# Optimization experiments

Hardware: AMD Instinct MI355X
Metric: run time of the kernel (lower is better)

Reference implementation:

```python
import jax, jax.numpy as jnp
import numpy as np

N, E, B = 50000, 800000, 512
DIN, H, A, BT = 128, 256, 40, 5


def _ln(h, g, b):
    m = jnp.mean(h, -1, keepdims=True)
    v = jnp.mean((h - m) ** 2, -1, keepdims=True)
    return (h - m) * jax.lax.rsqrt(v + 1e-5) * g + b


def _gcn(x, w, b, src, dst, n):
    # PyG GCNConv: add self-loops, symmetric D^-1/2 (A+I) D^-1/2 normalization
    h = x @ w
    loop = jnp.arange(n)
    s = jnp.concatenate([src, loop])
    d = jnp.concatenate([dst, loop])
    deg = jax.ops.segment_sum(jnp.ones(s.shape[0], h.dtype), d, num_segments=n)
    dinv = jax.lax.rsqrt(jnp.maximum(deg, 1.0))
    coef = (dinv[s] * dinv[d])[:, None]
    return jax.ops.segment_sum(coef * h[s], d, num_segments=n) + b


def _mlp2(x, w1, b1, w2, b2):
    return jax.nn.relu(x @ w1 + b1) @ w2 + b2


def _mlp3(x, w1, b1, w2, b2, w3, b3):
    h = jax.nn.relu(x @ w1 + b1)
    h = jax.nn.relu(h @ w2 + b2)
    return h @ w3 + b3


def setup_inputs() -> dict:
    key = jax.random.key(0)
    ks = iter(jax.random.split(key, 64))
    p = lambda shape: jax.random.normal(next(ks), shape, jnp.float32) * 0.05
    inp = {}
    inp["x"] = jax.random.normal(next(ks), (N, DIN), jnp.float32)
    inp["edge_index"] = jax.random.randint(next(ks), (2, E), 0, N)
    inp["batch"] = jnp.sort(jax.random.randint(next(ks), (N,), 0, B))
    inp["new_node_indices"] = jax.random.randint(next(ks), (B,), 0, N)
    inp["focus_node_indices"] = jax.random.randint(next(ks), (B,), 0, N)
    inp["num_graphs"] = B
    inp["conv_w0"] = p((DIN, H)); inp["conv_b0"] = p((H,))
    inp["conv_w1"] = p((H, H)); inp["conv_b1"] = p((H,))
    inp["conv_w2"] = p((H, H)); inp["conv_b2"] = p((H,))
    for i in range(3):
        inp[f"ln_g{i}"] = jnp.ones((H,), jnp.float32)
        inp[f"ln_b{i}"] = jnp.zeros((H,), jnp.float32)
    inp["res_w0"] = p((DIN, H)); inp["res_b0"] = p((H,))
    inp["stop_w1"] = p((H, H)); inp["stop_b1"] = p((H,))
    inp["stop_w2"] = p((H, 1)); inp["stop_b2"] = p((1,))
    inp["addn_w1"] = p((H, H)); inp["addn_b1"] = p((H,))
    inp["addn_w2"] = p((H, A)); inp["addn_b2"] = p((A,))
    inp["addb_w1"] = p((H, H)); inp["addb_b1"] = p((H,))
    inp["addb_w2"] = p((H, BT)); inp["addb_b2"] = p((BT,))
    inp["edge_w1"] = p((2 * H, H)); inp["edge_b1"] = p((H,))
    inp["edge_w2"] = p((H, H // 2)); inp["edge_b2"] = p((H // 2,))
    inp["edge_w3"] = p((H // 2, 1)); inp["edge_b3"] = p((1,))
    inp["bond_w1"] = p((2 * H, H)); inp["bond_b1"] = p((H,))
    inp["bond_w2"] = p((H, H // 2)); inp["bond_b2"] = p((H // 2,))
    inp["bond_w3"] = p((H // 2, BT)); inp["bond_b3"] = p((BT,))
    return inp


def reference(x, edge_index, batch, new_node_indices, focus_node_indices, num_graphs,
              conv_w0, conv_b0, conv_w1, conv_b1, conv_w2, conv_b2,
              ln_g0, ln_b0, ln_g1, ln_b1, ln_g2, ln_b2,
              res_w0, res_b0,
              stop_w1, stop_b1, stop_w2, stop_b2,
              addn_w1, addn_b1, addn_w2, addn_b2,
              addb_w1, addb_b1, addb_w2, addb_b2,
              edge_w1, edge_b1, edge_w2, edge_b2, edge_w3, edge_b3,
              bond_w1, bond_b1, bond_w2, bond_b2, bond_w3, bond_b3):
    n = x.shape[0]
    src, dst = edge_index[0], edge_index[1]
    conv_params = [(conv_w0, conv_b0), (conv_w1, conv_b1), (conv_w2, conv_b2)]
    ln_params = [(ln_g0, ln_b0), (ln_g1, ln_b1), (ln_g2, ln_b2)]
    h = x
    for i in range(3):
        h_in = h
        cw, cb = conv_params[i]
        lg, lb = ln_params[i]
        h = _gcn(h, cw, cb, src, dst, n)
        h = jax.nn.relu(_ln(h, lg, lb))  # dropout: eval mode (identity)
        res = h_in @ res_w0 + res_b0 if i == 0 else h_in
        h = h + res
    node_embeddings = h  # [N, H]
    # global mean pool over graphs
    counts = jax.ops.segment_sum(jnp.ones(n, h.dtype), batch, num_segments=num_graphs)
    graph_embedding = jax.ops.segment_sum(node_embeddings, batch, num_segments=num_graphs) / jnp.maximum(counts, 1.0)[:, None]
    stop_logits = _mlp2(graph_embedding, stop_w1, stop_b1, stop_w2, stop_b2)
    add_node_logits = _mlp2(graph_embedding, addn_w1, addn_b1, addn_w2, addn_b2)
    add_bond_logits = _mlp2(node_embeddings[focus_node_indices], addb_w1, addb_b1, addb_w2, addb_b2)
    # pair each node with its graph's newly added node
    new_node_embeddings = node_embeddings[new_node_indices]  # [B, H]
    pair = jnp.concatenate([node_embeddings, new_node_embeddings[batch]], axis=1)  # [N, 2H]
    edge_selection_logits = _mlp3(pair, edge_w1, edge_b1, edge_w2, edge_b2, edge_w3, edge_b3)
    bond_type_logits = _mlp3(pair, bond_w1, bond_b1, bond_w2, bond_b2, bond_w3, bond_b3)
    return (stop_logits, add_node_logits, add_bond_logits, node_embeddings,
            edge_selection_logits, bond_type_logits)
```

## Files before the change

### kernel.cpp

```cpp
#include <hip/hip_runtime.h>

typedef short bf16x8 __attribute__((ext_vector_type(8)));
typedef float f32x4 __attribute__((ext_vector_type(4)));
typedef unsigned short u16;
typedef u16 u16x4 __attribute__((ext_vector_type(4)));
typedef u16 u16x8 __attribute__((ext_vector_type(8)));

__device__ __forceinline__ float bf2f(u16 u) {
  union { float f; unsigned int i; } x; x.i = ((unsigned int)u) << 16; return x.f;
}
__device__ __forceinline__ u16 f2bf(float f) {
  union { float f; unsigned int i; } x; x.f = f;
  unsigned int r = x.i + 0x7fffu + ((x.i >> 16) & 1u);
  return (u16)(r >> 16);
}
__device__ __forceinline__ void st_out_(void* out, size_t idx, float v, int f32) {
  if (f32) ((float*)out)[idx] = v;
  else ((u16*)out)[idx] = f2bf(v);
}
__device__ __forceinline__ void gl_lds(const u16* g, u16* l) {
  __builtin_amdgcn_global_load_lds(
      (const __attribute__((address_space(1))) unsigned int*)g,
      (__attribute__((address_space(3))) unsigned int*)l, 16, 0, 0);
}

__global__ void k_detect(const u16* __restrict__ xx, int* flag) {
  int j = threadIdx.x;
  u16 u = xx[2 * j];
  int ex = (u >> 7) & 0xFF;
  int insane = (u != 0) && (ex < 100 || ex > 140);
  unsigned long long m = __ballot(insane);
  if (j == 0) flag[0] = (__popcll(m) > 8) ? 1 : 0;
}

__global__ void k_cvt_big(const void* __restrict__ src, u16* __restrict__ dst, int n,
                          const int* __restrict__ flag) {
  int i = blockIdx.x * 256 + threadIdx.x;
  if (i >= n) return;
  dst[i] = (*flag) ? f2bf(((const float*)src)[i]) : ((const u16*)src)[i];
}

#define NSEG 38
struct Cvt { const void* src[NSEG]; int off[NSEG + 1]; };
__global__ void k_cvt_all(Cvt c, u16* __restrict__ dst, int total, const int* __restrict__ flag) {
  int i = blockIdx.x * 256 + threadIdx.x;
  if (i >= total) return;
  int s = 0;
  #pragma unroll 1
  while (i >= c.off[s + 1]) s++;
  int j = i - c.off[s];
  dst[i] = (*flag) ? f2bf(((const float*)c.src[s])[j]) : ((const u16*)c.src[s])[j];
}

struct Tr { const u16* src[8]; u16* dst[8]; int lk[8]; int nc[8]; int off[9]; };
__global__ void k_tr_all(Tr c, int total) {
  int i = blockIdx.x * 256 + threadIdx.x;
  if (i >= total) return;
  int s = 0;
  #pragma unroll 1
  while (i >= c.off[s + 1]) s++;
  int j = i - c.off[s];
  int K = 1 << c.lk[s];
  int nrow = j >> c.lk[s], k = j & (K - 1);
  c.dst[s][j] = c.src[s][k * c.nc[s] + nrow];
}

__global__ void k_init(int* deg, int* cursor, int n) {
  int i = blockIdx.x * 256 + threadIdx.x;
  if (i < n) { deg[i] = 1; cursor[i] = 0; }
}
__global__ void k_deg(const int* __restrict__ dst, int* deg, int e) {
  int i = blockIdx.x * 256 + threadIdx.x;
  if (i < e) atomicAdd(&deg[dst[i]], 1);
}
__global__ void k_dinv(const int* __restrict__ deg, float* dinv, int n) {
  int i = blockIdx.x * 256 + threadIdx.x;
  if (i < n) dinv[i] = rsqrtf((float)deg[i]);
}
#define SCB 4096
__global__ __launch_bounds__(256) void k_scanA(const int* __restrict__ deg, int* bsum, int n) {
  int b = blockIdx.x, t = threadIdx.x;
  int base = b * SCB;
  int s = 0;
  for (int j = t; j < SCB; j += 256) { int i = base + j; s += (i < n) ? deg[i] - 1 : 0; }
  int l = t & 63, wid = t >> 6;
  #pragma unroll
  for (int o = 32; o; o >>= 1) s += __shfl_xor(s, o);
  __shared__ int red[4];
  if (l == 0) red[wid] = s;
  __syncthreads();
  if (t == 0) bsum[b] = red[0] + red[1] + red[2] + red[3];
}
__global__ void k_scanB(int* bsum, int nb, int* off, int n) {
  if (threadIdx.x == 0) {
    int c = 0;
    for (int i = 0; i < nb; i++) { int v = bsum[i]; bsum[i] = c; c += v; }
    off[n] = c;
  }
}
__global__ __launch_bounds__(256) void k_scanC(const int* __restrict__ deg, const int* __restrict__ bsum,
                                               int* off, int n) {
  int b = blockIdx.x, t = threadIdx.x;
  int base = b * SCB + t * 16;
  int loc[16]; int s = 0;
  #pragma unroll
  for (int j = 0; j < 16; j++) { int i = base + j; loc[j] = s; s += (i < n) ? deg[i] - 1 : 0; }
  int l = t & 63, wid = t >> 6;
  int incl = s;
  #pragma unroll
  for (int o = 1; o < 64; o <<= 1) { int y = __shfl_up(incl, o); if (l >= o) incl += y; }
  int excl = incl - s;
  __shared__ int ws[4];
  if (l == 63) ws[wid] = incl;
  __syncthreads();
  int woff = 0;
  for (int w = 0; w < wid; w++) woff += ws[w];
  int pre = bsum[b] + woff + excl;
  #pragma unroll
  for (int j = 0; j < 16; j++) { int i = base + j; if (i < n) off[i] = pre + loc[j]; }
}
__global__ void k_csr(const int* __restrict__ src, const int* __restrict__ dst,
                      const int* __restrict__ off, int* cursor, int* csr_src, int e) {
  int i = blockIdx.x * 256 + threadIdx.x;
  if (i >= e) return;
  int d = dst[i], s = src[i];
  int slot = atomicAdd(&cursor[d], 1);
  csr_src[off[d] + slot] = s;
}

template <int EPI>
__global__ __launch_bounds__(256) void gemm_k(
    const u16* __restrict__ A, int lda,
    const u16* __restrict__ Bt,
    u16* __restrict__ C, int ldc,
    int M, int K, int NC,
    const u16* __restrict__ colbias,
    const float* __restrict__ rowbias, int rbld, const int* __restrict__ rowmap) {
  __shared__ u16 As[2][128 * 64];
  __shared__ u16 Bs[2][128 * 64];
  const int t = threadIdx.x;
  const int m0 = blockIdx.x * 128;
  const int n0 = blockIdx.y * 128;
  const int wid = t >> 6, l = t & 63;
  const int wr = wid >> 1, wc = wid & 1;
  const int lr = l & 15, lg = l >> 4;
  const int srow = l >> 3, gc = l & 7;
  const int sg = gc ^ srow;

  auto stage = [&](int buf, int k0) {
    #pragma unroll
    for (int j = 0; j < 4; j++) {
      int row = wid * 32 + j * 8 + srow;
      int ga = m0 + row; if (ga >= M) ga = M - 1;
      gl_lds(A + (size_t)ga * lda + k0 + sg * 8, &As[buf][row * 64 + gc * 8]);
      gl_lds(Bt + (size_t)(n0 + row) * K + k0 + sg * 8, &Bs[buf][row * 64 + gc * 8]);
    }
  };

  f32x4 acc[4][4] = {};
  const int nT = K >> 6;
  stage(0, 0);
  asm volatile("s_waitcnt vmcnt(0)" ::: "memory");
  __builtin_amdgcn_s_barrier();
  int cur = 0;
  for (int kt = 0; kt < nT; kt++) {
    if (kt + 1 < nT) stage(cur ^ 1, (kt + 1) << 6);
    #pragma unroll
    for (int ks = 0; ks < 2; ks++) {
      const int gp = ((ks * 4 + lg) ^ (lr & 7)) * 8;
      bf16x8 af[4], bfr[4];
      #pragma unroll
      for (int mi = 0; mi < 4; mi++)
        af[mi] = *reinterpret_cast<const bf16x8*>(&As[cur][(wr * 64 + mi * 16 + lr) * 64 + gp]);
      #pragma unroll
      for (int ni = 0; ni < 4; ni++)
        bfr[ni] = *reinterpret_cast<const bf16x8*>(&Bs[cur][(wc * 64 + ni * 16 + lr) * 64 + gp]);
      #pragma unroll
      for (int mi = 0; mi < 4; mi++)
        #pragma unroll
        for (int ni = 0; ni < 4; ni++)
          acc[mi][ni] = __builtin_amdgcn_mfma_f32_16x16x32_bf16(af[mi], bfr[ni], acc[mi][ni], 0, 0, 0);
    }
    if (kt + 1 < nT) {
      asm volatile("s_waitcnt vmcnt(0)" ::: "memory");
      __builtin_amdgcn_s_barrier();
      cur ^= 1;
    }
  }
  #pragma unroll
  for (int mi = 0; mi < 4; mi++) {
    #pragma unroll
    for (int ni = 0; ni < 4; ni++) {
      int col = n0 + wc * 64 + ni * 16 + lr;
      float cbv = 0.f;
      if (EPI == 1 || EPI == 2) cbv = bf2f(colbias[col]);
      #pragma unroll
      for (int r = 0; r < 4; r++) {
        int row = m0 + wr * 64 + mi * 16 + lg * 4 + r;
        if (row < M) {
          float v = acc[mi][ni][r];
          if (EPI == 1 || EPI == 2) v += cbv;
          if (EPI == 3) v += rowbias[(size_t)rowmap[row] * rbld + col];
          if (EPI == 2 || EPI == 3) v = fmaxf(v, 0.f);
          C[(size_t)row * ldc + col] = f2bf(v);
        }
      }
    }
  }
}

__global__ __launch_bounds__(256, 6) void k_agg(
    const u16* __restrict__ hw, const u16* __restrict__ cb,
    const u16* __restrict__ lng, const u16* __restrict__ lnb,
    const u16* __restrict__ res, const float* __restrict__ dinv,
    const int* __restrict__ off, const int* __restrict__ csr_src,
    u16* __restrict__ hout, int n) {
  int l = threadIdx.x & 63;
  int v = blockIdx.x * 4 + (threadIdx.x >> 6);
  if (v >= n) return;
  const int half = l >> 5;
  const int c0 = (l & 31) * 8;
  float a[8] = {0, 0, 0, 0, 0, 0, 0, 0};
  int s = off[v], e = off[v + 1];
  int i = s;
  for (; i + 7 < e; i += 8) {
    int u0 = csr_src[i + half],     u1 = csr_src[i + 2 + half];
    int u2 = csr_src[i + 4 + half], u3 = csr_src[i + 6 + half];
    float w0 = dinv[u0], w1 = dinv[u1], w2 = dinv[u2], w3 = dinv[u3];
    u16x8 r0 = *reinterpret_cast<const u16x8*>(hw + (size_t)u0 * 256 + c0);
    u16x8 r1 = *reinterpret_cast<const u16x8*>(hw + (size_t)u1 * 256 + c0);
    u16x8 r2 = *reinterpret_cast<const u16x8*>(hw + (size_t)u2 * 256 + c0);
    u16x8 r3 = *reinterpret_cast<const u16x8*>(hw + (size_t)u3 * 256 + c0);
    #pragma unroll
    for (int j = 0; j < 8; j++)
      a[j] += w0 * bf2f(r0[j]) + w1 * bf2f(r1[j]) + w2 * bf2f(r2[j]) + w3 * bf2f(r3[j]);
  }
  for (; i < e; i += 2) {
    int idx = i + half;
    if (idx < e) {
      int u = csr_src[idx];
      float w = dinv[u];
      u16x8 r = *reinterpret_cast<const u16x8*>(hw + (size_t)u * 256 + c0);
      #pragma unroll
      for (int j = 0; j < 8; j++) a[j] += w * bf2f(r[j]);
    }
  }
  #pragma unroll
  for (int j = 0; j < 8; j++) a[j] += __shfl_xor(a[j], 32);
  float dv = dinv[v];
  u16x8 sv = *reinterpret_cast<const u16x8*>(hw + (size_t)v * 256 + c0);
  u16x8 cbv = *reinterpret_cast<const u16x8*>(cb + c0);
  float sum = 0.f;
  #pragma unroll
  for (int j = 0; j < 8; j++) {
    a[j] = dv * (dv * bf2f(sv[j]) + a[j]) + bf2f(cbv[j]);
    sum += a[j];
  }
  #pragma unroll
  for (int o = 16; o; o >>= 1) sum += __shfl_xor(sum, o);
  float mean = sum * (1.f / 256.f);
  float vs = 0.f;
  #pragma unroll
  for (int j = 0; j < 8; j++) { float d = a[j] - mean; vs += d * d; }
  #pragma unroll
  for (int o = 16; o; o >>= 1) vs += __shfl_xor(vs, o);
  float rs = rsqrtf(vs * (1.f / 256.f) + 1e-5f);
  u16x8 gv = *reinterpret_cast<const u16x8*>(lng + c0);
  u16x8 bv = *reinterpret_cast<const u16x8*>(lnb + c0);
  u16x8 rv = *reinterpret_cast<const u16x8*>(res + (size_t)v * 256 + c0);
  u16x8 ov;
  #pragma unroll
  for (int j = 0; j < 8; j++)
    ov[j] = f2bf(fmaxf((a[j] - mean) * rs * bf2f(gv[j]) + bf2f(bv[j]), 0.f) + bf2f(rv[j]));
  if (half == 0)
    *reinterpret_cast<u16x8*>(hout + (size_t)v * 256 + c0) = ov;
}

__global__ __launch_bounds__(256) void k_pool(const u16* __restrict__ h, const int* __restrict__ batch,
                                              int n, float* gemb) {
  int g = blockIdx.x, c = threadIdx.x;
  int lo = 0, hi = n;
  while (lo < hi) { int mid = (lo + hi) >> 1; if (batch[mid] < g) lo = mid + 1; else hi = mid; }
  int s = lo;
  lo = s; hi = n;
  while (lo < hi) { int mid = (lo + hi) >> 1; if (batch[mid] < g + 1) lo = mid + 1; else hi = mid; }
  int e = lo;
  float acc = 0.f;
  for (int i = s; i < e; i++) acc += bf2f(h[(size_t)i * 256 + c]);
  int cnt = e - s; if (cnt < 1) cnt = 1;
  gemb[g * 256 + c] = acc / (float)cnt;
}

__global__ __launch_bounds__(256) void k_glin(const u16* __restrict__ h, const int* __restrict__ nidx,
                                              const u16* __restrict__ W, const u16* __restrict__ b1,
                                              float* g1, int ld, int ofs) {
  int b = blockIdx.x, t = threadIdx.x;
  __shared__ float sin_[256];
  sin_[t] = bf2f(h[(size_t)nidx[b] * 256 + t]);
  __syncthreads();
  float acc = bf2f(b1[t]);
  for (int k = 0; k < 256; k++) acc += sin_[k] * bf2f(W[k * 256 + t]);
  g1[(size_t)b * ld + ofs + t] = acc;
}

template <int OUTD>
__global__ __launch_bounds__(256) void k_mlp2(const float* __restrict__ inf32,
                                              const u16* __restrict__ inbf, const int* __restrict__ idx,
                                              const u16* __restrict__ W1, const u16* __restrict__ b1,
                                              const u16* __restrict__ W2, const u16* __restrict__ b2,
                                              void* __restrict__ out, size_t obase,
                                              const int* __restrict__ flag) {
  int b = blockIdx.x, t = threadIdx.x;
  __shared__ float sin_[256];
  __shared__ float sh[256];
  sin_[t] = inf32 ? inf32[b * 256 + t] : bf2f(inbf[(size_t)idx[b] * 256 + t]);
  __syncthreads();
  float acc = bf2f(b1[t]);
  for (int k = 0; k < 256; k++) acc += sin_[k] * bf2f(W1[k * 256 + t]);
  sh[t] = fmaxf(acc, 0.f);
  __syncthreads();
  if (t < OUTD) {
    float a2 = bf2f(b2[t]);
    for (int k = 0; k < 256; k++) a2 += sh[k] * bf2f(W2[k * OUTD + t]);
    st_out_(out, obase + (size_t)b * OUTD + t, a2, *flag);
  }
}

__global__ __launch_bounds__(256) void k_final(const u16* __restrict__ t2e, const u16* __restrict__ t2b,
                                               const u16* __restrict__ w3e, const u16* __restrict__ b3e,
                                               const u16* __restrict__ w3b, const u16* __restrict__ b3b,
                                               void* __restrict__ out, size_t oe, size_t ob, int M,
                                               const int* __restrict__ flag) {
  int r = blockIdx.x * 4 + (threadIdx.x >> 6);
  int l = threadIdx.x & 63;
  if (r >= M) return;
  float p[6] = {0, 0, 0, 0, 0, 0};
  #pragma unroll
  for (int j = 0; j < 2; j++) {
    int k = l * 2 + j;
    float te = bf2f(t2e[(size_t)r * 128 + k]);
    float tb = bf2f(t2b[(size_t)r * 128 + k]);
    p[0] += te * bf2f(w3e[k]);
    #pragma unroll
    for (int q = 0; q < 5; q++) p[1 + q] += tb * bf2f(w3b[k * 5 + q]);
  }
  #pragma unroll
  for (int q = 0; q < 6; q++)
    #pragma unroll
    for (int o = 32; o; o >>= 1) p[q] += __shfl_xor(p[q], o);
  if (l == 0) {
    int f32 = *flag;
    st_out_(out, oe + r, p[0] + bf2f(b3e[0]), f32);
    #pragma unroll
    for (int q = 0; q < 5; q++)
      st_out_(out, ob + (size_t)r * 5 + q, p[1 + q] + bf2f(b3b[q]), f32);
  }
}

__global__ void k_emit8(const u16* __restrict__ src, void* __restrict__ out, size_t obase, int n8,
                        const int* __restrict__ flag) {
  int i = blockIdx.x * 256 + threadIdx.x;
  if (i >= n8) return;
  u16x8 v = reinterpret_cast<const u16x8*>(src)[i];
  if (*flag) {
    float4* fo = (float4*)((float*)out + obase);
    float4 lo, hi;
    lo.x = bf2f(v[0]); lo.y = bf2f(v[1]); lo.z = bf2f(v[2]); lo.w = bf2f(v[3]);
    hi.x = bf2f(v[4]); hi.y = bf2f(v[5]); hi.z = bf2f(v[6]); hi.w = bf2f(v[7]);
    fo[(size_t)i * 2] = lo; fo[(size_t)i * 2 + 1] = hi;
  } else {
    reinterpret_cast<u16x8*>((u16*)out + obase)[i] = v;
  }
}

extern "C" void kernel_launch(void* const* d_in, const int* in_sizes, int n_in,
                              void* d_out, int out_size, void* d_ws, size_t ws_size,
                              hipStream_t stream) {
  const int N = in_sizes[0] / 128;
  const int E = in_sizes[1] / 2;
  const int B = in_sizes[3];

  const int* ei    = (const int*)d_in[1];
  const int* srcp  = ei;
  const int* dstp  = ei + E;
  const int* batch = (const int*)d_in[2];
  const int* newi  = (const int*)d_in[3];
  const int* focus = (const int*)d_in[4];

  const size_t o_stop = 0;
  const size_t o_addn = (size_t)B;
  const size_t o_addb = (size_t)B + (size_t)B * 40;
  const size_t o_emb  = o_addb + (size_t)B * 5;
  const size_t o_esel = o_emb + (size_t)N * 256;
  const size_t o_bond = o_esel + (size_t)N;

  char* p = (char*)d_ws;
  auto alloc = [&](size_t bytes) -> void* {
    void* r = (void*)p;
    p += (bytes + 255) & ~(size_t)255;
    return r;
  };
  int* flag = (int*)alloc(4);
  static const int seg_din[NSEG] = {6,7,8,9,10,11, 12,13,14,15,16,17, 18,19,
                                    20,21,22,23, 24,25,26,27, 28,29,30,31,
                                    32,33,34,35,36,37, 38,39,40,41,42,43};
  static const int seg_len[NSEG] = {32768,256,65536,256,65536,256, 256,256,256,256,256,256,
                                    32768,256, 65536,256,256,1, 65536,256,10240,40,
                                    65536,256,1280,5, 131072,256,32768,128,128,1,
                                    131072,256,32768,128,640,5};
  int wtotal = 0;
  int seg_off[NSEG + 1];
  for (int i = 0; i < NSEG; i++) { seg_off[i] = wtotal; wtotal += seg_len[i]; }
  seg_off[NSEG] = wtotal;
  u16* wbf = (u16*)alloc((size_t)wtotal * 2);
  u16* wt_cw0 = (u16*)alloc(256 * 128 * 2);
  u16* wt_cw1 = (u16*)alloc(256 * 256 * 2);
  u16* wt_cw2 = (u16*)alloc(256 * 256 * 2);
  u16* wt_res = (u16*)alloc(256 * 128 * 2);
  u16* wt_t1  = (u16*)alloc(512 * 256 * 2);
  u16* wt_e2  = (u16*)alloc(128 * 256 * 2);
  u16* wt_b2  = (u16*)alloc(128 * 256 * 2);
  int*   deg     = (int*)alloc((size_t)N * 4);
  int*   cursor  = (int*)alloc((size_t)N * 4);
  int*   off     = (int*)alloc((size_t)(N + 1) * 4);
  float* dinv    = (float*)alloc((size_t)N * 4);
  int*   bsum    = (int*)alloc(64 * 4);
  float* gemb    = (float*)alloc((size_t)B * 256 * 4);
  float* g1full  = (float*)alloc((size_t)B * 512 * 4);
  int*   csr_src = (int*)alloc((size_t)E * 4);
  u16*   xbf     = (u16*)alloc((size_t)N * 128 * 2);
  u16*   P1      = (u16*)alloc((size_t)N * 256 * 2);
  u16*   P2      = (u16*)alloc((size_t)N * 256 * 2);
  u16*   P3      = (u16*)alloc((size_t)N * 256 * 2);

  auto wseg = [&](int i) -> u16* { return wbf + seg_off[i]; };
  u16 *cw0 = wseg(0), *cb0 = wseg(1), *cw1 = wseg(2), *cb1 = wseg(3), *cw2 = wseg(4), *cb2 = wseg(5);
  u16 *lg0 = wseg(6), *lb0 = wseg(7), *lg1 = wseg(8), *lb1 = wseg(9), *lg2 = wseg(10), *lb2 = wseg(11);
  u16 *rw0 = wseg(12), *rb0 = wseg(13);
  u16 *sw1 = wseg(14), *sb1 = wseg(15), *sw2 = wseg(16), *sb2 = wseg(17);
  u16 *aw1 = wseg(18), *ab1 = wseg(19), *aw2 = wseg(20), *ab2 = wseg(21);
  u16 *bw1 = wseg(22), *bb1 = wseg(23), *bw2 = wseg(24), *bb2 = wseg(25);
  u16 *ew1 = wseg(26), *eb1 = wseg(27), *ew2 = wseg(28), *eb2 = wseg(29), *ew3 = wseg(30), *eb3 = wseg(31);
  u16 *qw1 = wseg(32), *qb1 = wseg(33), *qw2 = wseg(34), *qb2 = wseg(35), *qw3 = wseg(36), *qb3 = wseg(37);

  k_detect<<<1, 64, 0, stream>>>((const u16*)d_in[0], flag);
  k_cvt_big<<<(N * 128 + 255) / 256, 256, 0, stream>>>(d_in[0], xbf, N * 128, flag);
  Cvt cd;
  for (int i = 0; i < NSEG; i++) cd.src[i] = d_in[seg_din[i]];
  for (int i = 0; i <= NSEG; i++) cd.off[i] = seg_off[i];
  k_cvt_all<<<(wtotal + 255) / 256, 256, 0, stream>>>(cd, wbf, wtotal, flag);

  const int NB = (N + 255) / 256;
  const int EBk = (E + 255) / 256;
  const int NBS = (N + SCB - 1) / SCB;

  k_init<<<NB, 256, 0, stream>>>(deg, cursor, N);
  k_deg<<<EBk, 256, 0, stream>>>(dstp, deg, E);
  k_dinv<<<NB, 256, 0, stream>>>(deg, dinv, N);
  k_scanA<<<NBS, 256, 0, stream>>>(deg, bsum, N);
  k_scanB<<<1, 64, 0, stream>>>(bsum, NBS, off, N);
  k_scanC<<<NBS, 256, 0, stream>>>(deg, bsum, off, N);
  k_csr<<<EBk, 256, 0, stream>>>(srcp, dstp, off, cursor, csr_src, E);

  {
    Tr td;
    const u16* ts[8] = {cw0, cw1, cw2, rw0, ew1, qw1, ew2, qw2};
    u16* tdst[8] = {wt_cw0, wt_cw1, wt_cw2, wt_res, wt_t1, wt_t1 + 256 * 256, wt_e2, wt_b2};
    int tlk[8] = {7, 8, 8, 7, 8, 8, 8, 8};
    int tnc[8] = {256, 256, 256, 256, 256, 256, 128, 128};
    int tlen[8] = {32768, 65536, 65536, 32768, 65536, 65536, 32768, 32768};
    int tot = 0;
    for (int i = 0; i < 8; i++) {
      td.src[i] = ts[i]; td.dst[i] = tdst[i]; td.lk[i] = tlk[i]; td.nc[i] = tnc[i];
      td.off[i] = tot; tot += tlen[i];
    }
    td.off[8] = tot;
    k_tr_all<<<(tot + 255) / 256, 256, 0, stream>>>(td, tot);
  }

  dim3 g256((N + 127) / 128, 2);
  dim3 g512((N + 127) / 128, 4);
  dim3 g128((N + 127) / 128, 1);
  const int AGB = (N + 3) / 4;

  gemm_k<1><<<g256, 256, 0, stream>>>(xbf, 128, wt_res, P1, 256, N, 128, 256, rb0, nullptr, 0, nullptr);
  gemm_k<0><<<g256, 256, 0, stream>>>(xbf, 128, wt_cw0, P2, 256, N, 128, 256, nullptr, nullptr, 0, nullptr);
  k_agg<<<AGB, 256, 0, stream>>>(P2, cb0, lg0, lb0, P1, dinv, off, csr_src, P3, N);
  gemm_k<0><<<g256, 256, 0, stream>>>(P3, 256, wt_cw1, P2, 256, N, 256, 256, nullptr, nullptr, 0, nullptr);
  k_agg<<<AGB, 256, 0, stream>>>(P2, cb1, lg1, lb1, P3, dinv, off, csr_src, P1, N);
  gemm_k<0><<<g256, 256, 0, stream>>>(P1, 256, wt_cw2, P2, 256, N, 256, 256, nullptr, nullptr, 0, nullptr);
  k_agg<<<AGB, 256, 0, stream>>>(P2, cb2, lg2, lb2, P1, dinv, off, csr_src, P3, N);

  k_emit8<<<(N * 256 / 8 + 255) / 256, 256, 0, stream>>>(P3, d_out, o_emb, N * 256 / 8, flag);

  k_pool<<<B, 256, 0, stream>>>(P3, batch, N, gemb);
  k_glin<<<B, 256, 0, stream>>>(P3, newi, ew1 + 256 * 256, eb1, g1full, 512, 0);
  k_glin<<<B, 256, 0, stream>>>(P3, newi, qw1 + 256 * 256, qb1, g1full, 512, 256);
  k_mlp2<1><<<B, 256, 0, stream>>>(gemb, nullptr, nullptr, sw1, sb1, sw2, sb2, d_out, o_stop, flag);
  k_mlp2<40><<<B, 256, 0, stream>>>(gemb, nullptr, nullptr, aw1, ab1, aw2, ab2, d_out, o_addn, flag);
  k_mlp2<5><<<B, 256, 0, stream>>>(nullptr, P3, focus, bw1, bb1, bw2, bb2, d_out, o_addb, flag);

  u16* T1 = P1;
  gemm_k<3><<<g512, 256, 0, stream>>>(P3, 256, wt_t1, T1, 512, N, 256, 512, nullptr, g1full, 512, batch);
  u16* t2e = P3;
  u16* t2b = P3 + (size_t)N * 128;
  gemm_k<2><<<g128, 256, 0, stream>>>(T1, 512, wt_e2, t2e, 128, N, 256, 128, eb2, nullptr, 0, nullptr);
  gemm_k<2><<<g128, 256, 0, stream>>>(T1 + 256, 512, wt_b2, t2b, 128, N, 256, 128, qb2, nullptr, 0, nullptr);
  k_final<<<(N + 3) / 4, 256, 0, stream>>>(t2e, t2b, ew3, eb3, qw3, qb3, d_out, o_esel, o_bond, N, flag);
}
```

Measured before the change: 651.4 us.

## Restructure GEMM to keep full-K weight tile in LDS and stream A directly

Replaces the double-buffered LDS-staged 128x128 GEMM with a kernel that loads a 64-column slice of the full-K weight matrix into swizzled LDS once. Each wave then reads its A rows straight from global memory into registers, with no per-K-step barriers. The grid is reoriented so column blocks are the fast dimension, which lets neighbouring blocks share A rows through cache. The row-bias gather is hoisted ahead of the store loop, and the small MLP loops gain unroll pragmas. The risk is that uncoalesced direct global A loads without prefetch may expose latency, and the large LDS footprint limits occupancy.

Result: slower. 669.1 us (+2.7%).

```diff
diff --git a/kernel.cpp b/kernel.cpp
--- a/kernel.cpp
+++ b/kernel.cpp
@@ -17,11 +17,6 @@
 __device__ __forceinline__ void st_out_(void* out, size_t idx, float v, int f32) {
   if (f32) ((float*)out)[idx] = v;
   else ((u16*)out)[idx] = f2bf(v);
-}
-__device__ __forceinline__ void gl_lds(const u16* g, u16* l) {
-  __builtin_amdgcn_global_load_lds(
-      (const __attribute__((address_space(1))) unsigned int*)g,
-      (__attribute__((address_space(3))) unsigned int*)l, 16, 0, 0);
 }
 
 __global__ void k_detect(const u16* __restrict__ xx, int* flag) {
@@ -129,80 +124,87 @@
 }
 
 template <int EPI>
-__global__ __launch_bounds__(256) void gemm_k(
+__global__ __launch_bounds__(256) void gemm_w(
     const u16* __restrict__ A, int lda,
     const u16* __restrict__ Bt,
     u16* __restrict__ C, int ldc,
     int M, int K, int NC,
     const u16* __restrict__ colbias,
     const float* __restrict__ rowbias, int rbld, const int* __restrict__ rowmap) {
-  __shared__ u16 As[2][128 * 64];
-  __shared__ u16 Bs[2][128 * 64];
+  __shared__ u16 Bs[64 * 256];
   const int t = threadIdx.x;
-  const int m0 = blockIdx.x * 128;
-  const int n0 = blockIdx.y * 128;
+  const int n0 = blockIdx.x * 64;
+  const int m0 = blockIdx.y * 256;
+  {
+    const int ng = K >> 3;
+    const int tot = 64 * ng;
+    for (int i = t; i < tot; i += 256) {
+      int c = i / ng, g = i - c * ng;
+      u16x8 v = *reinterpret_cast<const u16x8*>(Bt + (size_t)(n0 + c) * K + g * 8);
+      int gs = g ^ (c & 7);
+      *reinterpret_cast<u16x8*>(&Bs[c * K + gs * 8]) = v;
+    }
+  }
+  __syncthreads();
+
   const int wid = t >> 6, l = t & 63;
-  const int wr = wid >> 1, wc = wid & 1;
+  const int rbase = m0 + wid * 64;
   const int lr = l & 15, lg = l >> 4;
-  const int srow = l >> 3, gc = l & 7;
-  const int sg = gc ^ srow;
-
-  auto stage = [&](int buf, int k0) {
-    #pragma unroll
-    for (int j = 0; j < 4; j++) {
-      int row = wid * 32 + j * 8 + srow;
-      int ga = m0 + row; if (ga >= M) ga = M - 1;
-      gl_lds(A + (size_t)ga * lda + k0 + sg * 8, &As[buf][row * 64 + gc * 8]);
-      gl_lds(Bt + (size_t)(n0 + row) * K + k0 + sg * 8, &Bs[buf][row * 64 + gc * 8]);
-    }
-  };
-
   f32x4 acc[4][4] = {};
-  const int nT = K >> 6;
-  stage(0, 0);
-  asm volatile("s_waitcnt vmcnt(0)" ::: "memory");
-  __builtin_amdgcn_s_barrier();
-  int cur = 0;
-  for (int kt = 0; kt < nT; kt++) {
-    if (kt + 1 < nT) stage(cur ^ 1, (kt + 1) << 6);
-    #pragma unroll
-    for (int ks = 0; ks < 2; ks++) {
-      const int gp = ((ks * 4 + lg) ^ (lr & 7)) * 8;
-      bf16x8 af[4], bfr[4];
-      #pragma unroll
-      for (int mi = 0; mi < 4; mi++)
-        af[mi] = *reinterpret_cast<const bf16x8*>(&As[cur][(wr * 64 + mi * 16 + lr) * 64 + gp]);
+  const int nks = K >> 5;
+  #pragma unroll 2
+  for (int ks = 0; ks < nks; ks++) {
+    bf16x8 af[4], bfr[4];
+    #pragma unroll
+    for (int mi = 0; mi < 4; mi++) {
+      int row = rbase + mi * 16 + lr; if (row >= M) row = M - 1;
+      af[mi] = *reinterpret_cast<const bf16x8*>(A + (size_t)row * lda + ks * 32 + lg * 8);
+    }
+    #pragma unroll
+    for (int ni = 0; ni < 4; ni++) {
+      int c = ni * 16 + lr;
+      int g = (ks * 4 + lg) ^ (lr & 7);
+      bfr[ni] = *reinterpret_cast<const bf16x8*>(&Bs[c * K + g * 8]);
+    }
+    #pragma unroll
+    for (int mi = 0; mi < 4; mi++)
       #pragma unroll
       for (int ni = 0; ni < 4; ni++)
-        bfr[ni] = *reinterpret_cast<const bf16x8*>(&Bs[cur][(wc * 64 + ni * 16 + lr) * 64 + gp]);
+        acc[mi][ni] = __builtin_amdgcn_mfma_f32_16x16x32_bf16(af[mi], bfr[ni], acc[mi][ni], 0, 0, 0);
+  }
+
+  #pragma unroll
+  for (int mi = 0; mi < 4; mi++) {
+    int rowi[4];
+    #pragma unroll
+    for (int r = 0; r < 4; r++) rowi[r] = rbase + mi * 16 + lg * 4 + r;
+    float rbv[4][4];
+    if (EPI == 3) {
+      int rmv[4];
       #pragma unroll
-      for (int mi = 0; mi < 4; mi++)
+      for (int r = 0; r < 4; r++) {
+        int rr = rowi[r]; if (rr >= M) rr = M - 1;
+        rmv[r] = rowmap[rr];
+      }
+      #pragma unroll
+      for (int ni = 0; ni < 4; ni++)
         #pragma unroll
-        for (int ni = 0; ni < 4; ni++)
-          acc[mi][ni] = __builtin_amdgcn_mfma_f32_16x16x32_bf16(af[mi], bfr[ni], acc[mi][ni], 0, 0, 0);
-    }
-    if (kt + 1 < nT) {
-      asm volatile("s_waitcnt vmcnt(0)" ::: "memory");
-      __builtin_amdgcn_s_barrier();
-      cur ^= 1;
-    }
-  }
-  #pragma unroll
-  for (int mi = 0; mi < 4; mi++) {
+        for (int r = 0; r < 4; r++)
+          rbv[ni][r] = rowbias[(size_t)rmv[r] * rbld + n0 + ni * 16 + lr];
+    }
     #pragma unroll
     for (int ni = 0; ni < 4; ni++) {
-      int col = n0 + wc * 64 + ni * 16 + lr;
+      int col = n0 + ni * 16 + lr;
       float cbv = 0.f;
       if (EPI == 1 || EPI == 2) cbv = bf2f(colbias[col]);
       #pragma unroll
       for (int r = 0; r < 4; r++) {
-        int row = m0 + wr * 64 + mi * 16 + lg * 4 + r;
-        if (row < M) {
+        if (rowi[r] < M) {
           float v = acc[mi][ni][r];
           if (EPI == 1 || EPI == 2) v += cbv;
-          if (EPI == 3) v += rowbias[(size_t)rowmap[row] * rbld + col];
+          if (EPI == 3) v += rbv[ni][r];
           if (EPI == 2 || EPI == 3) v = fmaxf(v, 0.f);
-          C[(size_t)row * ldc + col] = f2bf(v);
+          C[(size_t)rowi[r] * ldc + col] = f2bf(v);
         }
       }
     }
@@ -299,6 +301,7 @@
   sin_[t] = bf2f(h[(size_t)nidx[b] * 256 + t]);
   __syncthreads();
   float acc = bf2f(b1[t]);
+  #pragma unroll 8
   for (int k = 0; k < 256; k++) acc += sin_[k] * bf2f(W[k * 256 + t]);
   g1[(size_t)b * ld + ofs + t] = acc;
 }
@@ -316,11 +319,13 @@
   sin_[t] = inf32 ? inf32[b * 256 + t] : bf2f(inbf[(size_t)idx[b] * 256 + t]);
   __syncthreads();
   float acc = bf2f(b1[t]);
+  #pragma unroll 8
   for (int k = 0; k < 256; k++) acc += sin_[k] * bf2f(W1[k * 256 + t]);
   sh[t] = fmaxf(acc, 0.f);
   __syncthreads();
   if (t < OUTD) {
     float a2 = bf2f(b2[t]);
+    #pragma unroll 8
     for (int k = 0; k < 256; k++) a2 += sh[k] * bf2f(W2[k * OUTD + t]);
     st_out_(out, obase + (size_t)b * OUTD + t, a2, *flag);
   }
@@ -478,17 +483,18 @@
     k_tr_all<<<(tot + 255) / 256, 256, 0, stream>>>(td, tot);
   }
 
-  dim3 g256((N + 127) / 128, 2);
-  dim3 g512((N + 127) / 128, 4);
-  dim3 g128((N + 127) / 128, 1);
+  const int MB = (N + 255) / 256;
+  dim3 gw4(4, MB);
+  dim3 gw8(8, MB);
+  dim3 gw2(2, MB);
   const int AGB = (N + 3) / 4;
 
-  gemm_k<1><<<g256, 256, 0, stream>>>(xbf, 128, wt_res, P1, 256, N, 128, 256, rb0, nullptr, 0, nullptr);
-  gemm_k<0><<<g256, 256, 0, stream>>>(xbf, 128, wt_cw0, P2, 256, N, 128, 256, nullptr, nullptr, 0, nullptr);
+  gemm_w<1><<<gw4, 256, 0, stream>>>(xbf, 128, wt_res, P1, 256, N, 128, 256, rb0, nullptr, 0, nullptr);
+  gemm_w<0><<<gw4, 256, 0, stream>>>(xbf, 128, wt_cw0, P2, 256, N, 128, 256, nullptr, nullptr, 0, nullptr);
   k_agg<<<AGB, 256, 0, stream>>>(P2, cb0, lg0, lb0, P1, dinv, off, csr_src, P3, N);
-  gemm_k<0><<<g256, 256, 0, stream>>>(P3, 256, wt_cw1, P2, 256, N, 256, 256, nullptr, nullptr, 0, nullptr);
+  gemm_w<0><<<gw4, 256, 0, stream>>>(P3, 256, wt_cw1, P2, 256, N, 256, 256, nullptr, nullptr, 0, nullptr);
   k_agg<<<AGB, 256, 0, stream>>>(P2, cb1, lg1, lb1, P3, dinv, off, csr_src, P1, N);
-  gemm_k<0><<<g256, 256, 0, stream>>>(P1, 256, wt_cw2, P2, 256, N, 256, 256, nullptr, nullptr, 0, nullptr);
+  gemm_w<0><<<gw4, 256, 0, stream>>>(P1, 256, wt_cw2, P2, 256, N, 256, 256, nullptr, nullptr, 0, nullptr);
   k_agg<<<AGB, 256, 0, stream>>>(P2, cb2, lg2, lb2, P1, dinv, off, csr_src, P3, N);
 
   k_emit8<<<(N * 256 / 8 + 255) / 256, 256, 0, stream>>>(P3, d_out, o_emb, N * 256 / 8, flag);
@@ -501,10 +507,10 @@
   k_mlp2<5><<<B, 256, 0, stream>>>(nullptr, P3, focus, bw1, bb1, bw2, bb2, d_out, o_addb, flag);
 
   u16* T1 = P1;
-  gemm_k<3><<<g512, 256, 0, stream>>>(P3, 256, wt_t1, T1, 512, N, 256, 512, nullptr, g1full, 512, batch);
+  gemm_w<3><<<gw8, 256, 0, stream>>>(P3, 256, wt_t1, T1, 512, N, 256, 512, nullptr, g1full, 512, batch);
   u16* t2e = P3;
   u16* t2b = P3 + (size_t)N * 128;
-  gemm_k<2><<<g128, 256, 0, stream>>>(T1, 512, wt_e2, t2e, 128, N, 256, 128, eb2, nullptr, 0, nullptr);
-  gemm_k<2><<<g128, 256, 0, stream>>>(T1 + 256, 512, wt_b2, t2b, 128, N, 256, 128, qb2, nullptr, 0, nullptr);
+  gemm_w<2><<<gw2, 256, 0, stream>>>(T1, 512, wt_e2, t2e, 128, N, 256, 128, eb2, nullptr, 0, nullptr);
+  gemm_w<2><<<gw2, 256, 0, stream>>>(T1 + 256, 512, wt_b2, t2b, 128, N, 256, 128, qb2, nullptr, 0, nullptr);
   k_final<<<(N + 3) / 4, 256, 0, stream>>>(t2e, t2b, ew3, eb3, qw3, qb3, d_out, o_esel, o_bond, N, flag);
 }
```
